# Kernel optimization log

Measured on AMD Instinct MI355X. Metric: run time of the kernel, lower is better.

The kernel has to match this reference:

```python
import jax, jax.numpy as jnp
import numpy as np

IN_CHS = 128
NUM_HEADS = 4
WIN = 7
N = WIN * WIN            # 49 tokens per window
QKDIM = 128              # ceil(in_chs/num_groups/num_heads)*num_heads
HEAD_DIM = QKDIM // NUM_HEADS
SCALE = HEAD_DIM ** -0.5
B = 4096                 # batch * num_windows


def _relative_position_index(win_h, win_w):
    coords = np.stack(np.meshgrid(np.arange(win_h), np.arange(win_w), indexing='ij'))  # [2,h,w]
    cf = coords.reshape(2, -1)                      # [2, N]
    rc = (cf[:, :, None] - cf[:, None, :]).transpose(1, 2, 0).astype(np.int64)  # [N,N,2]
    rc[:, :, 0] += win_h - 1
    rc[:, :, 1] += win_w - 1
    rc[:, :, 0] *= 2 * win_w - 1
    return rc.sum(-1)                               # [N, N]


def setup_inputs() -> dict:
    key = jax.random.key(0)
    ks = jax.random.split(key, 8)
    x = jax.random.normal(ks[0], (B, N, IN_CHS), dtype=jnp.float32)
    qk_w = jax.random.normal(ks[1], (2 * QKDIM, IN_CHS), dtype=jnp.float32) * 0.02
    qk_b = jnp.zeros((2 * QKDIM,), dtype=jnp.float32)
    v_w = jax.random.normal(ks[2], (IN_CHS, IN_CHS), dtype=jnp.float32) * 0.02
    v_b = jnp.zeros((IN_CHS,), dtype=jnp.float32)
    proj_w = jax.random.normal(ks[3], (IN_CHS, IN_CHS), dtype=jnp.float32) * 0.02
    proj_b = jnp.zeros((IN_CHS,), dtype=jnp.float32)
    bias_table = jax.random.normal(ks[4], ((2 * WIN - 1) * (2 * WIN - 1), NUM_HEADS), dtype=jnp.float32) * 0.02
    rel_idx = jnp.asarray(_relative_position_index(WIN, WIN))  # [N,N] int64
    return {"x": x, "qk_w": qk_w, "qk_b": qk_b, "v_w": v_w, "v_b": v_b,
            "proj_w": proj_w, "proj_b": proj_b, "bias_table": bias_table,
            "rel_idx": rel_idx}


def reference(x, qk_w, qk_b, v_w, v_b, proj_w, proj_b, bias_table, rel_idx):
    Bn, Nn, C = x.shape
    # fused q/k projection: [B,N,2*qkdim] -> q,k each [B,H,N,d]
    qk = (x @ qk_w.T + qk_b).reshape(Bn, Nn, 2, NUM_HEADS, HEAD_DIM)
    q = qk[:, :, 0].transpose(0, 2, 1, 3)
    k = qk[:, :, 1].transpose(0, 2, 1, 3)
    v = (x @ v_w.T + v_b).reshape(Bn, Nn, NUM_HEADS, -1).transpose(0, 2, 1, 3)
    # windowed QK^T with gathered relative-position bias
    attn = jnp.einsum('bhnd,bhmd->bhnm', q * SCALE, k)
    bias = bias_table[rel_idx.reshape(-1)].reshape(Nn, Nn, NUM_HEADS).transpose(2, 0, 1)
    attn = jax.nn.softmax(attn + bias[None], axis=-1)
    out = jnp.einsum('bhnm,bhmd->bhnd', attn, v).transpose(0, 2, 1, 3).reshape(Bn, Nn, -1)
    return out @ proj_w.T + proj_b
```

## Files before the change

### kernel.cpp

```cpp
#include <hip/hip_runtime.h>
#include <hip/hip_bf16.h>

typedef __attribute__((ext_vector_type(8))) __bf16 bf16x8;
typedef __attribute__((ext_vector_type(4))) float f32x4;

#define MFMA(a,b,c) __builtin_amdgcn_mfma_f32_16x16x32_bf16((a),(b),(c),0,0,0)

#define XB 0u
#define QB 16384u
#define KB 32768u
#define VT 49152u

static __device__ __forceinline__ unsigned short f2u(float x) {
  return __builtin_bit_cast(unsigned short, static_cast<__bf16>(x));
}
static __device__ __forceinline__ unsigned long long pack4(float a, float b, float c, float d) {
  union { __bf16 h[4]; unsigned long long u; } z;
  z.h[0] = static_cast<__bf16>(a);
  z.h[1] = static_cast<__bf16>(b);
  z.h[2] = static_cast<__bf16>(c);
  z.h[3] = static_cast<__bf16>(d);
  return z.u;
}
static __device__ __forceinline__ unsigned long long pack4v(f32x4 v) {
  return pack4(v[0], v[1], v[2], v[3]);
}
static __device__ __forceinline__ unsigned sw256(unsigned row, unsigned colb) {
  return (row << 8) + (colb ^ ((row & 7u) << 4));
}
static __device__ __forceinline__ unsigned sw128(unsigned row, unsigned colb) {
  return (row << 7) + (colb ^ ((row & 7u) << 4));
}

__global__ void rsa_prep(const float* __restrict__ qk_w, const float* __restrict__ v_w,
                         const float* __restrict__ proj_w, const float* __restrict__ bias_table,
                         unsigned short* __restrict__ wqk, unsigned short* __restrict__ wv,
                         unsigned short* __restrict__ wp, float* __restrict__ biasNN) {
  const float SCALE = 0.17677669529663687f;
  int t = blockIdx.x * blockDim.x + threadIdx.x;
  int stride = gridDim.x * blockDim.x;
  for (int i = t; i < 256 * 128; i += stride) {
    float v = qk_w[i];
    if (i < 128 * 128) v *= SCALE;
    wqk[i] = f2u(v);
  }
  for (int i = t; i < 128 * 128; i += stride) wv[i] = f2u(v_w[i]);
  for (int i = t; i < 128 * 128; i += stride) wp[i] = f2u(proj_w[i]);
  for (int i = t; i < 4 * 64 * 64; i += stride) {
    int h = i >> 12, r = (i >> 6) & 63, m = i & 63;
    float v = -1e9f;
    if (r < 49 && m < 49) {
      int ri = r / 7, rj = r - ri * 7, mi = m / 7, mj = m - mi * 7;
      int rel = (ri - mi + 6) * 13 + (rj - mj + 6);
      v = bias_table[rel * 4 + h];
    }
    biasNN[i] = v;
  }
}

__global__ __launch_bounds__(512, 4) void rsa_main(
    const float* __restrict__ x, const float* __restrict__ qk_bias,
    const float* __restrict__ v_bias, const float* __restrict__ proj_bias,
    const unsigned short* __restrict__ wqk, const unsigned short* __restrict__ wv,
    const unsigned short* __restrict__ wp, const float* __restrict__ biasNN,
    float* __restrict__ out) {
  __shared__ __align__(16) unsigned char LDS[65536];
  const int tid = threadIdx.x;
  const int w = tid >> 6;
  const int lane = tid & 63;
  const int c = lane & 15;
  const int g = lane >> 4;
  const int b = blockIdx.x;
  const float SCALE = 0.17677669529663687f;

  {
    const f32x4* xp = reinterpret_cast<const f32x4*>(x + (size_t)b * 6272);
    for (int i = tid; i < 1568; i += 512) {
      f32x4 v = xp[i];
      unsigned row = (unsigned)i >> 5, c4 = (unsigned)i & 31u;
      *reinterpret_cast<unsigned long long*>(LDS + XB + sw256(row, c4 * 8)) = pack4v(v);
    }
    for (int i = tid; i < 480; i += 512) {
      unsigned row = 49 + ((unsigned)i >> 5), c4 = (unsigned)i & 31u;
      *reinterpret_cast<unsigned long long*>(LDS + XB + sw256(row, c4 * 8)) = 0ull;
    }
  }
  __syncthreads();

  __builtin_amdgcn_s_setprio(1);
#pragma unroll
  for (int mi = 0; mi < 2; ++mi) {
    const int mt = w + 8 * mi;
    bf16x8 a[4];
    const unsigned short* wrow = wqk + (mt * 16 + c) * 128 + g * 8;
#pragma unroll
    for (int ks = 0; ks < 4; ++ks) a[ks] = *reinterpret_cast<const bf16x8*>(wrow + ks * 32);
    const int chout = mt * 16 + g * 4;
    f32x4 bias4 = *reinterpret_cast<const f32x4*>(qk_bias + chout);
    if (mi == 0) { bias4[0] *= SCALE; bias4[1] *= SCALE; bias4[2] *= SCALE; bias4[3] *= SCALE; }
#pragma unroll
    for (int nt = 0; nt < 4; ++nt) {
      f32x4 acc = {0.f, 0.f, 0.f, 0.f};
#pragma unroll
      for (int ks = 0; ks < 4; ++ks) {
        bf16x8 bf = *reinterpret_cast<const bf16x8*>(LDS + XB + sw256(nt * 16 + c, (ks * 32 + g * 8) * 2));
        acc = MFMA(a[ks], bf, acc);
      }
      const unsigned tok = nt * 16 + c;
      const unsigned colb = ((mt & 7) * 16 + g * 4) * 2;
      const unsigned base = (mi == 0) ? QB : KB;
      *reinterpret_cast<unsigned long long*>(LDS + base + sw256(tok, colb)) =
          pack4(acc[0] + bias4[0], acc[1] + bias4[1], acc[2] + bias4[2], acc[3] + bias4[3]);
    }
  }

  {
    const float vb = v_bias[w * 16 + c];
    bf16x8 bw[4];
    const unsigned short* wrow = wv + (w * 16 + c) * 128 + g * 8;
#pragma unroll
    for (int ks = 0; ks < 4; ++ks) bw[ks] = *reinterpret_cast<const bf16x8*>(wrow + ks * 32);
#pragma unroll
    for (int mt = 0; mt < 4; ++mt) {
      f32x4 acc = {0.f, 0.f, 0.f, 0.f};
#pragma unroll
      for (int ks = 0; ks < 4; ++ks) {
        bf16x8 af = *reinterpret_cast<const bf16x8*>(LDS + XB + sw256(mt * 16 + c, (ks * 32 + g * 8) * 2));
        acc = MFMA(af, bw[ks], acc);
      }
      const unsigned row = w * 16 + c;
      const unsigned colb = (mt * 16 + g * 4) * 2;
      *reinterpret_cast<unsigned long long*>(LDS + VT + sw128(row, colb)) =
          pack4(acc[0] + vb, acc[1] + vb, acc[2] + vb, acc[3] + vb);
    }
  }
  __builtin_amdgcn_s_setprio(0);
  __syncthreads();

  const int h = w >> 1;
  const int rt0 = (w & 1) * 2;

  f32x4 bb[2][4];
#pragma unroll
  for (int r2 = 0; r2 < 2; ++r2) {
    const int r = (rt0 + r2) * 16 + c;
    const float* bp = biasNN + ((h * 64 + r) << 6);
#pragma unroll
    for (int mt = 0; mt < 4; ++mt)
      bb[r2][mt] = *reinterpret_cast<const f32x4*>(bp + mt * 16 + g * 4);
  }

  f32x4 s[2][4];
  __builtin_amdgcn_s_setprio(1);
#pragma unroll
  for (int r2 = 0; r2 < 2; ++r2) {
    const int rt = rt0 + r2;
    bf16x8 qf = *reinterpret_cast<const bf16x8*>(LDS + QB + sw256(rt * 16 + c, h * 64 + g * 16));
#pragma unroll
    for (int mt = 0; mt < 4; ++mt) {
      bf16x8 kf = *reinterpret_cast<const bf16x8*>(LDS + KB + sw256(mt * 16 + c, h * 64 + g * 16));
      f32x4 z = {0.f, 0.f, 0.f, 0.f};
      s[r2][mt] = MFMA(kf, qf, z);
    }
  }
  __builtin_amdgcn_s_setprio(0);
  __syncthreads();

#pragma unroll
  for (int r2 = 0; r2 < 2; ++r2) {
    const int r = (rt0 + r2) * 16 + c;
    float v[16];
    float sum = 0.f;
#pragma unroll
    for (int mt = 0; mt < 4; ++mt) {
#pragma unroll
      for (int j = 0; j < 4; ++j) {
        v[mt * 4 + j] = __expf(s[r2][mt][j] + bb[r2][mt][j]);
        sum += v[mt * 4 + j];
      }
    }
    sum += __shfl_xor(sum, 16);
    sum += __shfl_xor(sum, 32);
    const float inv = (sum > 0.f) ? 1.0f / sum : 0.f;
#pragma unroll
    for (int mt = 0; mt < 4; ++mt)
      *reinterpret_cast<unsigned long long*>(LDS + QB + h * 8192 + sw128(r, (mt * 16 + g * 4) * 2)) =
          pack4(v[mt * 4] * inv, v[mt * 4 + 1] * inv, v[mt * 4 + 2] * inv, v[mt * 4 + 3] * inv);
  }

#pragma unroll
  for (int dt = 0; dt < 2; ++dt) {
#pragma unroll
    for (int r2 = 0; r2 < 2; ++r2) {
      const int r = (rt0 + r2) * 16 + c;
      f32x4 acc = {0.f, 0.f, 0.f, 0.f};
#pragma unroll
      for (int ks = 0; ks < 2; ++ks) {
        bf16x8 af = *reinterpret_cast<const bf16x8*>(LDS + VT + sw128(h * 32 + dt * 16 + c, (ks * 32 + g * 8) * 2));
        bf16x8 pf = *reinterpret_cast<const bf16x8*>(LDS + QB + h * 8192 + sw128(r, (ks * 32 + g * 8) * 2));
        acc = MFMA(af, pf, acc);
      }
      *reinterpret_cast<unsigned long long*>(LDS + XB + sw256(r, (h * 32 + dt * 16 + g * 4) * 2)) = pack4v(acc);
    }
  }
  __syncthreads();

  {
    bf16x8 ap[4];
    const unsigned short* wrow = wp + (w * 16 + c) * 128 + g * 8;
#pragma unroll
    for (int ks = 0; ks < 4; ++ks) ap[ks] = *reinterpret_cast<const bf16x8*>(wrow + ks * 32);
    f32x4 pb4 = *reinterpret_cast<const f32x4*>(proj_bias + w * 16 + g * 4);
    __builtin_amdgcn_s_setprio(1);
#pragma unroll
    for (int nt = 0; nt < 4; ++nt) {
      f32x4 acc = {0.f, 0.f, 0.f, 0.f};
#pragma unroll
      for (int ks = 0; ks < 4; ++ks) {
        bf16x8 bf = *reinterpret_cast<const bf16x8*>(LDS + XB + sw256(nt * 16 + c, (ks * 32 + g * 8) * 2));
        acc = MFMA(ap[ks], bf, acc);
      }
      const int tok = nt * 16 + c;
      if (tok < 49) {
        f32x4 o = {acc[0] + pb4[0], acc[1] + pb4[1], acc[2] + pb4[2], acc[3] + pb4[3]};
        *reinterpret_cast<f32x4*>(out + ((size_t)b * 49 + tok) * 128 + w * 16 + g * 4) = o;
      }
    }
    __builtin_amdgcn_s_setprio(0);
  }
}

extern "C" void kernel_launch(void* const* d_in, const int* in_sizes, int n_in,
                              void* d_out, int out_size, void* d_ws, size_t ws_size,
                              hipStream_t stream) {
  const float* x          = (const float*)d_in[0];
  const float* qk_w       = (const float*)d_in[1];
  const float* qk_b       = (const float*)d_in[2];
  const float* v_w        = (const float*)d_in[3];
  const float* v_b        = (const float*)d_in[4];
  const float* proj_w     = (const float*)d_in[5];
  const float* proj_b     = (const float*)d_in[6];
  const float* bias_table = (const float*)d_in[7];
  float* out = (float*)d_out;

  unsigned short* wqk = (unsigned short*)d_ws;
  unsigned short* wv  = wqk + 256 * 128;
  unsigned short* wp  = wv + 128 * 128;
  float* biasNN = (float*)((char*)d_ws + 131072);

  const int B = in_sizes[0] / (49 * 128);

  rsa_prep<<<dim3(128), dim3(512), 0, stream>>>(qk_w, v_w, proj_w, bias_table, wqk, wv, wp, biasNN);
  rsa_main<<<dim3(B), dim3(512), 0, stream>>>(x, qk_b, v_b, proj_b, wqk, wv, wp, biasNN, out);
}
```

Baseline: 123.0 us.

## Process two windows per block with register prefetch of next window's input

Each block now handles two windows in sequence, halving the grid. The next window's x tile is loaded into registers while the current window computes, so global load latency overlaps with MFMA work. PV operand fragments are now loaded up front before their MFMAs. Launch bounds drop from 4 to 2 waves per SIMD, which allows more registers but lowers occupancy. The extra per-window barriers and the smaller grid of 2048 blocks may reduce latency hiding.

```diff
diff --git a/kernel.cpp b/kernel.cpp
--- a/kernel.cpp
+++ b/kernel.cpp
@@ -58,175 +58,199 @@
   }
 }
 
-__global__ __launch_bounds__(512, 4) void rsa_main(
+__global__ __launch_bounds__(512, 2) void rsa_main(
     const float* __restrict__ x, const float* __restrict__ qk_bias,
     const float* __restrict__ v_bias, const float* __restrict__ proj_bias,
     const unsigned short* __restrict__ wqk, const unsigned short* __restrict__ wv,
     const unsigned short* __restrict__ wp, const float* __restrict__ biasNN,
-    float* __restrict__ out) {
+    float* __restrict__ out, int Btot) {
   __shared__ __align__(16) unsigned char LDS[65536];
   const int tid = threadIdx.x;
   const int w = tid >> 6;
   const int lane = tid & 63;
   const int c = lane & 15;
   const int g = lane >> 4;
-  const int b = blockIdx.x;
-  const float SCALE = 0.17677669529663687f;
-
-  {
-    const f32x4* xp = reinterpret_cast<const f32x4*>(x + (size_t)b * 6272);
-    for (int i = tid; i < 1568; i += 512) {
-      f32x4 v = xp[i];
-      unsigned row = (unsigned)i >> 5, c4 = (unsigned)i & 31u;
-      *reinterpret_cast<unsigned long long*>(LDS + XB + sw256(row, c4 * 8)) = pack4v(v);
-    }
-    for (int i = tid; i < 480; i += 512) {
-      unsigned row = 49 + ((unsigned)i >> 5), c4 = (unsigned)i & 31u;
-      *reinterpret_cast<unsigned long long*>(LDS + XB + sw256(row, c4 * 8)) = 0ull;
-    }
-  }
-  __syncthreads();
-
-  __builtin_amdgcn_s_setprio(1);
-#pragma unroll
-  for (int mi = 0; mi < 2; ++mi) {
-    const int mt = w + 8 * mi;
-    bf16x8 a[4];
-    const unsigned short* wrow = wqk + (mt * 16 + c) * 128 + g * 8;
-#pragma unroll
-    for (int ks = 0; ks < 4; ++ks) a[ks] = *reinterpret_cast<const bf16x8*>(wrow + ks * 32);
-    const int chout = mt * 16 + g * 4;
-    f32x4 bias4 = *reinterpret_cast<const f32x4*>(qk_bias + chout);
-    if (mi == 0) { bias4[0] *= SCALE; bias4[1] *= SCALE; bias4[2] *= SCALE; bias4[3] *= SCALE; }
-#pragma unroll
-    for (int nt = 0; nt < 4; ++nt) {
-      f32x4 acc = {0.f, 0.f, 0.f, 0.f};
-#pragma unroll
-      for (int ks = 0; ks < 4; ++ks) {
-        bf16x8 bf = *reinterpret_cast<const bf16x8*>(LDS + XB + sw256(nt * 16 + c, (ks * 32 + g * 8) * 2));
-        acc = MFMA(a[ks], bf, acc);
-      }
-      const unsigned tok = nt * 16 + c;
-      const unsigned colb = ((mt & 7) * 16 + g * 4) * 2;
-      const unsigned base = (mi == 0) ? QB : KB;
-      *reinterpret_cast<unsigned long long*>(LDS + base + sw256(tok, colb)) =
-          pack4(acc[0] + bias4[0], acc[1] + bias4[1], acc[2] + bias4[2], acc[3] + bias4[3]);
-    }
-  }
-
-  {
-    const float vb = v_bias[w * 16 + c];
-    bf16x8 bw[4];
-    const unsigned short* wrow = wv + (w * 16 + c) * 128 + g * 8;
-#pragma unroll
-    for (int ks = 0; ks < 4; ++ks) bw[ks] = *reinterpret_cast<const bf16x8*>(wrow + ks * 32);
-#pragma unroll
-    for (int mt = 0; mt < 4; ++mt) {
-      f32x4 acc = {0.f, 0.f, 0.f, 0.f};
-#pragma unroll
-      for (int ks = 0; ks < 4; ++ks) {
-        bf16x8 af = *reinterpret_cast<const bf16x8*>(LDS + XB + sw256(mt * 16 + c, (ks * 32 + g * 8) * 2));
-        acc = MFMA(af, bw[ks], acc);
-      }
-      const unsigned row = w * 16 + c;
-      const unsigned colb = (mt * 16 + g * 4) * 2;
-      *reinterpret_cast<unsigned long long*>(LDS + VT + sw128(row, colb)) =
-          pack4(acc[0] + vb, acc[1] + vb, acc[2] + vb, acc[3] + vb);
-    }
-  }
-  __builtin_amdgcn_s_setprio(0);
-  __syncthreads();
-
   const int h = w >> 1;
   const int rt0 = (w & 1) * 2;
-
-  f32x4 bb[2][4];
-#pragma unroll
-  for (int r2 = 0; r2 < 2; ++r2) {
-    const int r = (rt0 + r2) * 16 + c;
-    const float* bp = biasNN + ((h * 64 + r) << 6);
-#pragma unroll
-    for (int mt = 0; mt < 4; ++mt)
-      bb[r2][mt] = *reinterpret_cast<const f32x4*>(bp + mt * 16 + g * 4);
-  }
-
-  f32x4 s[2][4];
-  __builtin_amdgcn_s_setprio(1);
-#pragma unroll
-  for (int r2 = 0; r2 < 2; ++r2) {
-    const int rt = rt0 + r2;
-    bf16x8 qf = *reinterpret_cast<const bf16x8*>(LDS + QB + sw256(rt * 16 + c, h * 64 + g * 16));
-#pragma unroll
-    for (int mt = 0; mt < 4; ++mt) {
-      bf16x8 kf = *reinterpret_cast<const bf16x8*>(LDS + KB + sw256(mt * 16 + c, h * 64 + g * 16));
-      f32x4 z = {0.f, 0.f, 0.f, 0.f};
-      s[r2][mt] = MFMA(kf, qf, z);
-    }
-  }
-  __builtin_amdgcn_s_setprio(0);
-  __syncthreads();
-
-#pragma unroll
-  for (int r2 = 0; r2 < 2; ++r2) {
-    const int r = (rt0 + r2) * 16 + c;
-    float v[16];
-    float sum = 0.f;
-#pragma unroll
-    for (int mt = 0; mt < 4; ++mt) {
-#pragma unroll
-      for (int j = 0; j < 4; ++j) {
-        v[mt * 4 + j] = __expf(s[r2][mt][j] + bb[r2][mt][j]);
-        sum += v[mt * 4 + j];
-      }
-    }
-    sum += __shfl_xor(sum, 16);
-    sum += __shfl_xor(sum, 32);
-    const float inv = (sum > 0.f) ? 1.0f / sum : 0.f;
-#pragma unroll
-    for (int mt = 0; mt < 4; ++mt)
-      *reinterpret_cast<unsigned long long*>(LDS + QB + h * 8192 + sw128(r, (mt * 16 + g * 4) * 2)) =
-          pack4(v[mt * 4] * inv, v[mt * 4 + 1] * inv, v[mt * 4 + 2] * inv, v[mt * 4 + 3] * inv);
-  }
-
-#pragma unroll
-  for (int dt = 0; dt < 2; ++dt) {
+  const float SCALE = 0.17677669529663687f;
+
+  const int b0 = blockIdx.x * 2;
+  if (b0 >= Btot) return;
+  const int nw = (Btot - b0 < 2) ? (Btot - b0) : 2;
+
+  f32x4 xr[4];
+  {
+    const f32x4* xp = reinterpret_cast<const f32x4*>(x + (size_t)b0 * 6272);
+#pragma unroll
+    for (int j = 0; j < 3; ++j) xr[j] = xp[tid + j * 512];
+    xr[3] = (tid < 32) ? xp[tid + 1536] : f32x4{0.f, 0.f, 0.f, 0.f};
+  }
+
+  for (int i = 0; i < nw; ++i) {
+    const int b = b0 + i;
+    if (i) __syncthreads();
+
+#pragma unroll
+    for (int j = 0; j < 4; ++j) {
+      unsigned idx = (unsigned)tid + (unsigned)j * 512u;
+      unsigned row = idx >> 5, c4 = idx & 31u;
+      *reinterpret_cast<unsigned long long*>(LDS + XB + sw256(row, c4 * 8)) = pack4v(xr[j]);
+    }
+    __syncthreads();
+
+    if (i + 1 < nw) {
+      const f32x4* xp = reinterpret_cast<const f32x4*>(x + (size_t)(b0 + 1) * 6272);
+#pragma unroll
+      for (int j = 0; j < 3; ++j) xr[j] = xp[tid + j * 512];
+      if (tid < 32) xr[3] = xp[tid + 1536];
+    }
+
+    __builtin_amdgcn_s_setprio(1);
+#pragma unroll
+    for (int mi = 0; mi < 2; ++mi) {
+      const int mt = w + 8 * mi;
+      bf16x8 a[4];
+      const unsigned short* wrow = wqk + (mt * 16 + c) * 128 + g * 8;
+#pragma unroll
+      for (int ks = 0; ks < 4; ++ks) a[ks] = *reinterpret_cast<const bf16x8*>(wrow + ks * 32);
+      const int chout = mt * 16 + g * 4;
+      f32x4 bias4 = *reinterpret_cast<const f32x4*>(qk_bias + chout);
+      if (mi == 0) { bias4[0] *= SCALE; bias4[1] *= SCALE; bias4[2] *= SCALE; bias4[3] *= SCALE; }
+#pragma unroll
+      for (int nt = 0; nt < 4; ++nt) {
+        f32x4 acc = {0.f, 0.f, 0.f, 0.f};
+#pragma unroll
+        for (int ks = 0; ks < 4; ++ks) {
+          bf16x8 bf = *reinterpret_cast<const bf16x8*>(LDS + XB + sw256(nt * 16 + c, (ks * 32 + g * 8) * 2));
+          acc = MFMA(a[ks], bf, acc);
+        }
+        const unsigned tok = nt * 16 + c;
+        const unsigned colb = ((mt & 7) * 16 + g * 4) * 2;
+        const unsigned base = (mi == 0) ? QB : KB;
+        *reinterpret_cast<unsigned long long*>(LDS + base + sw256(tok, colb)) =
+            pack4(acc[0] + bias4[0], acc[1] + bias4[1], acc[2] + bias4[2], acc[3] + bias4[3]);
+      }
+    }
+
+    {
+      const float vb = v_bias[w * 16 + c];
+      bf16x8 bw[4];
+      const unsigned short* wrow = wv + (w * 16 + c) * 128 + g * 8;
+#pragma unroll
+      for (int ks = 0; ks < 4; ++ks) bw[ks] = *reinterpret_cast<const bf16x8*>(wrow + ks * 32);
+#pragma unroll
+      for (int mt = 0; mt < 4; ++mt) {
+        f32x4 acc = {0.f, 0.f, 0.f, 0.f};
+#pragma unroll
+        for (int ks = 0; ks < 4; ++ks) {
+          bf16x8 af = *reinterpret_cast<const bf16x8*>(LDS + XB + sw256(mt * 16 + c, (ks * 32 + g * 8) * 2));
+          acc = MFMA(af, bw[ks], acc);
+        }
+        const unsigned row = w * 16 + c;
+        const unsigned colb = (mt * 16 + g * 4) * 2;
+        *reinterpret_cast<unsigned long long*>(LDS + VT + sw128(row, colb)) =
+            pack4(acc[0] + vb, acc[1] + vb, acc[2] + vb, acc[3] + vb);
+      }
+    }
+    __builtin_amdgcn_s_setprio(0);
+    __syncthreads();
+
+    f32x4 bb[2][4];
 #pragma unroll
     for (int r2 = 0; r2 < 2; ++r2) {
       const int r = (rt0 + r2) * 16 + c;
-      f32x4 acc = {0.f, 0.f, 0.f, 0.f};
-#pragma unroll
-      for (int ks = 0; ks < 2; ++ks) {
-        bf16x8 af = *reinterpret_cast<const bf16x8*>(LDS + VT + sw128(h * 32 + dt * 16 + c, (ks * 32 + g * 8) * 2));
-        bf16x8 pf = *reinterpret_cast<const bf16x8*>(LDS + QB + h * 8192 + sw128(r, (ks * 32 + g * 8) * 2));
-        acc = MFMA(af, pf, acc);
-      }
-      *reinterpret_cast<unsigned long long*>(LDS + XB + sw256(r, (h * 32 + dt * 16 + g * 4) * 2)) = pack4v(acc);
-    }
-  }
-  __syncthreads();
-
-  {
-    bf16x8 ap[4];
-    const unsigned short* wrow = wp + (w * 16 + c) * 128 + g * 8;
-#pragma unroll
-    for (int ks = 0; ks < 4; ++ks) ap[ks] = *reinterpret_cast<const bf16x8*>(wrow + ks * 32);
-    f32x4 pb4 = *reinterpret_cast<const f32x4*>(proj_bias + w * 16 + g * 4);
+      const float* bp = biasNN + ((h * 64 + r) << 6);
+#pragma unroll
+      for (int mt = 0; mt < 4; ++mt)
+        bb[r2][mt] = *reinterpret_cast<const f32x4*>(bp + mt * 16 + g * 4);
+    }
+
+    f32x4 s[2][4];
     __builtin_amdgcn_s_setprio(1);
 #pragma unroll
-    for (int nt = 0; nt < 4; ++nt) {
-      f32x4 acc = {0.f, 0.f, 0.f, 0.f};
-#pragma unroll
-      for (int ks = 0; ks < 4; ++ks) {
-        bf16x8 bf = *reinterpret_cast<const bf16x8*>(LDS + XB + sw256(nt * 16 + c, (ks * 32 + g * 8) * 2));
-        acc = MFMA(ap[ks], bf, acc);
-      }
-      const int tok = nt * 16 + c;
-      if (tok < 49) {
-        f32x4 o = {acc[0] + pb4[0], acc[1] + pb4[1], acc[2] + pb4[2], acc[3] + pb4[3]};
-        *reinterpret_cast<f32x4*>(out + ((size_t)b * 49 + tok) * 128 + w * 16 + g * 4) = o;
+    for (int r2 = 0; r2 < 2; ++r2) {
+      const int rt = rt0 + r2;
+      bf16x8 qf = *reinterpret_cast<const bf16x8*>(LDS + QB + sw256(rt * 16 + c, h * 64 + g * 16));
+#pragma unroll
+      for (int mt = 0; mt < 4; ++mt) {
+        bf16x8 kf = *reinterpret_cast<const bf16x8*>(LDS + KB + sw256(mt * 16 + c, h * 64 + g * 16));
+        f32x4 z = {0.f, 0.f, 0.f, 0.f};
+        s[r2][mt] = MFMA(kf, qf, z);
       }
     }
     __builtin_amdgcn_s_setprio(0);
+    __syncthreads();
+
+#pragma unroll
+    for (int r2 = 0; r2 < 2; ++r2) {
+      const int r = (rt0 + r2) * 16 + c;
+      float v[16];
+      float sum = 0.f;
+#pragma unroll
+      for (int mt = 0; mt < 4; ++mt) {
+#pragma unroll
+        for (int j = 0; j < 4; ++j) {
+          v[mt * 4 + j] = __expf(s[r2][mt][j] + bb[r2][mt][j]);
+          sum += v[mt * 4 + j];
+        }
+      }
+      sum += __shfl_xor(sum, 16);
+      sum += __shfl_xor(sum, 32);
+      const float inv = (sum > 0.f) ? 1.0f / sum : 0.f;
+#pragma unroll
+      for (int mt = 0; mt < 4; ++mt)
+        *reinterpret_cast<unsigned long long*>(LDS + QB + h * 8192 + sw128(r, (mt * 16 + g * 4) * 2)) =
+            pack4(v[mt * 4] * inv, v[mt * 4 + 1] * inv, v[mt * 4 + 2] * inv, v[mt * 4 + 3] * inv);
+    }
+
+    {
+      bf16x8 af[2][2], pf[2][2];
+#pragma unroll
+      for (int dt = 0; dt < 2; ++dt)
+#pragma unroll
+        for (int ks = 0; ks < 2; ++ks)
+          af[dt][ks] = *reinterpret_cast<const bf16x8*>(LDS + VT + sw128(h * 32 + dt * 16 + c, (ks * 32 + g * 8) * 2));
+#pragma unroll
+      for (int r2 = 0; r2 < 2; ++r2)
+#pragma unroll
+        for (int ks = 0; ks < 2; ++ks)
+          pf[r2][ks] = *reinterpret_cast<const bf16x8*>(LDS + QB + h * 8192 + sw128((rt0 + r2) * 16 + c, (ks * 32 + g * 8) * 2));
+#pragma unroll
+      for (int dt = 0; dt < 2; ++dt)
+#pragma unroll
+        for (int r2 = 0; r2 < 2; ++r2) {
+          const int r = (rt0 + r2) * 16 + c;
+          f32x4 acc = {0.f, 0.f, 0.f, 0.f};
+          acc = MFMA(af[dt][0], pf[r2][0], acc);
+          acc = MFMA(af[dt][1], pf[r2][1], acc);
+          *reinterpret_cast<unsigned long long*>(LDS + XB + sw256(r, (h * 32 + dt * 16 + g * 4) * 2)) = pack4v(acc);
+        }
+    }
+    __syncthreads();
+
+    {
+      bf16x8 ap[4];
+      const unsigned short* wrow = wp + (w * 16 + c) * 128 + g * 8;
+#pragma unroll
+      for (int ks = 0; ks < 4; ++ks) ap[ks] = *reinterpret_cast<const bf16x8*>(wrow + ks * 32);
+      f32x4 pb4 = *reinterpret_cast<const f32x4*>(proj_bias + w * 16 + g * 4);
+      __builtin_amdgcn_s_setprio(1);
+#pragma unroll
+      for (int nt = 0; nt < 4; ++nt) {
+        f32x4 acc = {0.f, 0.f, 0.f, 0.f};
+#pragma unroll
+        for (int ks = 0; ks < 4; ++ks) {
+          bf16x8 bf = *reinterpret_cast<const bf16x8*>(LDS + XB + sw256(nt * 16 + c, (ks * 32 + g * 8) * 2));
+          acc = MFMA(ap[ks], bf, acc);
+        }
+        const int tok = nt * 16 + c;
+        if (tok < 49) {
+          f32x4 o = {acc[0] + pb4[0], acc[1] + pb4[1], acc[2] + pb4[2], acc[3] + pb4[3]};
+          *reinterpret_cast<f32x4*>(out + ((size_t)b * 49 + tok) * 128 + w * 16 + g * 4) = o;
+        }
+      }
+      __builtin_amdgcn_s_setprio(0);
+    }
   }
 }
 
@@ -249,7 +273,8 @@
   float* biasNN = (float*)((char*)d_ws + 131072);
 
   const int B = in_sizes[0] / (49 * 128);
+  const int grid = (B + 1) / 2;
 
   rsa_prep<<<dim3(128), dim3(512), 0, stream>>>(qk_w, v_w, proj_w, bias_table, wqk, wv, wp, biasNN);
-  rsa_main<<<dim3(B), dim3(512), 0, stream>>>(x, qk_b, v_b, proj_b, wqk, wv, wp, biasNN, out);
-}
+  rsa_main<<<dim3(grid), dim3(512), 0, stream>>>(x, qk_b, v_b, proj_b, wqk, wv, wp, biasNN, out, B);
+}
```

Result: slower. 132.1 us (+7.4%).

## Keep softmax probabilities in registers and feed PV via 16x16x16 MFMA

Applied to the files above, without the earlier changes.

The softmax output no longer round-trips through LDS. Normalized probabilities are packed into registers in the layout of the 16x16x16 bf16 MFMA B-operand, and the PV product uses that instruction directly against V fragments read from LDS. This removes one LDS write/read pass and one __syncthreads barrier. The proj weight and bias loads are also hoisted earlier so they overlap with this work. The cost is more register pressure and twice as many smaller-K MFMA instructions for the PV step.

```diff
diff --git a/kernel.cpp b/kernel.cpp
--- a/kernel.cpp
+++ b/kernel.cpp
@@ -2,9 +2,11 @@
 #include <hip/hip_bf16.h>
 
 typedef __attribute__((ext_vector_type(8))) __bf16 bf16x8;
+typedef __attribute__((ext_vector_type(4))) short short4v;
 typedef __attribute__((ext_vector_type(4))) float f32x4;
 
 #define MFMA(a,b,c) __builtin_amdgcn_mfma_f32_16x16x32_bf16((a),(b),(c),0,0,0)
+#define MFMA16(a,b,c) __builtin_amdgcn_mfma_f32_16x16x16bf16_1k((a),(b),(c),0,0,0)
 
 #define XB 0u
 #define QB 16384u
@@ -24,6 +26,14 @@
 }
 static __device__ __forceinline__ unsigned long long pack4v(f32x4 v) {
   return pack4(v[0], v[1], v[2], v[3]);
+}
+static __device__ __forceinline__ short4v pack4s(float a, float b, float c, float d) {
+  union { __bf16 h[4]; short4v s; } z;
+  z.h[0] = static_cast<__bf16>(a);
+  z.h[1] = static_cast<__bf16>(b);
+  z.h[2] = static_cast<__bf16>(c);
+  z.h[3] = static_cast<__bf16>(d);
+  return z.s;
 }
 static __device__ __forceinline__ unsigned sw256(unsigned row, unsigned colb) {
   return (row << 8) + (colb ^ ((row & 7u) << 4));
@@ -164,11 +174,10 @@
     }
   }
   __builtin_amdgcn_s_setprio(0);
-  __syncthreads();
-
+
+  short4v pk[2][4];
 #pragma unroll
   for (int r2 = 0; r2 < 2; ++r2) {
-    const int r = (rt0 + r2) * 16 + c;
     float v[16];
     float sum = 0.f;
 #pragma unroll
@@ -184,33 +193,51 @@
     const float inv = (sum > 0.f) ? 1.0f / sum : 0.f;
 #pragma unroll
     for (int mt = 0; mt < 4; ++mt)
-      *reinterpret_cast<unsigned long long*>(LDS + QB + h * 8192 + sw128(r, (mt * 16 + g * 4) * 2)) =
-          pack4(v[mt * 4] * inv, v[mt * 4 + 1] * inv, v[mt * 4 + 2] * inv, v[mt * 4 + 3] * inv);
-  }
-
-#pragma unroll
-  for (int dt = 0; dt < 2; ++dt) {
+      pk[r2][mt] = pack4s(v[mt * 4] * inv, v[mt * 4 + 1] * inv,
+                          v[mt * 4 + 2] * inv, v[mt * 4 + 3] * inv);
+  }
+
+  f32x4 od[2][2];
+  {
+    short4v vfrag[2][4];
+#pragma unroll
+    for (int ct2 = 0; ct2 < 2; ++ct2)
+#pragma unroll
+      for (int ks = 0; ks < 4; ++ks)
+        vfrag[ct2][ks] = *reinterpret_cast<const short4v*>(
+            LDS + VT + sw128((h * 2 + ct2) * 16 + c, (ks * 16 + g * 4) * 2));
+    __builtin_amdgcn_s_setprio(1);
+#pragma unroll
+    for (int ct2 = 0; ct2 < 2; ++ct2)
+#pragma unroll
+      for (int r2 = 0; r2 < 2; ++r2) {
+        f32x4 acc = {0.f, 0.f, 0.f, 0.f};
+#pragma unroll
+        for (int ks = 0; ks < 4; ++ks) acc = MFMA16(vfrag[ct2][ks], pk[r2][ks], acc);
+        od[ct2][r2] = acc;
+      }
+    __builtin_amdgcn_s_setprio(0);
+  }
+
+  bf16x8 ap[4];
+  {
+    const unsigned short* wrow = wp + (w * 16 + c) * 128 + g * 8;
+#pragma unroll
+    for (int ks = 0; ks < 4; ++ks) ap[ks] = *reinterpret_cast<const bf16x8*>(wrow + ks * 32);
+  }
+  f32x4 pb4 = *reinterpret_cast<const f32x4*>(proj_bias + w * 16 + g * 4);
+
+#pragma unroll
+  for (int ct2 = 0; ct2 < 2; ++ct2)
 #pragma unroll
     for (int r2 = 0; r2 < 2; ++r2) {
       const int r = (rt0 + r2) * 16 + c;
-      f32x4 acc = {0.f, 0.f, 0.f, 0.f};
-#pragma unroll
-      for (int ks = 0; ks < 2; ++ks) {
-        bf16x8 af = *reinterpret_cast<const bf16x8*>(LDS + VT + sw128(h * 32 + dt * 16 + c, (ks * 32 + g * 8) * 2));
-        bf16x8 pf = *reinterpret_cast<const bf16x8*>(LDS + QB + h * 8192 + sw128(r, (ks * 32 + g * 8) * 2));
-        acc = MFMA(af, pf, acc);
-      }
-      *reinterpret_cast<unsigned long long*>(LDS + XB + sw256(r, (h * 32 + dt * 16 + g * 4) * 2)) = pack4v(acc);
-    }
-  }
+      *reinterpret_cast<unsigned long long*>(
+          LDS + XB + sw256(r, ((h * 2 + ct2) * 16 + g * 4) * 2)) = pack4v(od[ct2][r2]);
+    }
   __syncthreads();
 
   {
-    bf16x8 ap[4];
-    const unsigned short* wrow = wp + (w * 16 + c) * 128 + g * 8;
-#pragma unroll
-    for (int ks = 0; ks < 4; ++ks) ap[ks] = *reinterpret_cast<const bf16x8*>(wrow + ks * 32);
-    f32x4 pb4 = *reinterpret_cast<const f32x4*>(proj_bias + w * 16 + g * 4);
     __builtin_amdgcn_s_setprio(1);
 #pragma unroll
     for (int nt = 0; nt < 4; ++nt) {
```

New measurement: 119.2 us. 3.1% less time.
